# Kernel tuning notes

Hardware: AMD Instinct MI355X
Metric: run time of the kernel (lower is better)

Reference implementation:

```python
import jax, jax.numpy as jnp
import numpy as np
import math

N_STATIONS = 50  # N in [N, 7, 56] causal matrix


def setup_inputs() -> dict:
    key = jax.random.key(0)
    k1, k2, k3, k4 = jax.random.split(key, 4)
    B, L, H, E = 3200, 7, 8, 64
    S, D = 56, 64
    queries = jax.random.normal(k1, (B, L, H, E), dtype=jnp.float32)
    keys = jax.random.normal(k2, (B, S, H, E), dtype=jnp.float32)
    values = jax.random.normal(k3, (B, S, H, D), dtype=jnp.float32)
    # station-specific multiplicative causal matrix in [0, 1]
    attn_mask = jax.random.uniform(k4, (N_STATIONS, L, S), dtype=jnp.float32)
    return {"queries": queries, "keys": keys, "values": values, "attn_mask": attn_mask}


def reference(queries, keys, values, attn_mask):
    B, L, H, E = queries.shape
    S = values.shape[1]
    N = attn_mask.shape[0]  # number of stations; B % N == 0
    ab = B // N  # actual batch size per station group
    scale = 1.0 / math.sqrt(E)
    # raw scores [B, H, L, S]
    scores = jnp.einsum('blhe,bshe->bhls', queries, keys)
    # multiplicative station-specific mask: reshape batch into (ab, N) and
    # broadcast mask [N, L, S] over (ab, H)
    masked = scores.reshape(ab, N, H, L, S) * attn_mask[None, :, None, :, :]
    masked = masked.reshape(B, H, L, S)
    # note: scale is applied AFTER masking, as in the original module
    A = jax.nn.softmax(scale * masked, axis=-1)  # dropout is identity at eval
    V = jnp.einsum('bhls,bshd->blhd', A, values)
    return V
```

## Files before the change

### kernel.cpp

```cpp
#include <hip/hip_runtime.h>
#include <math.h>


__launch_bounds__(64)
__global__ void fullattn_kernel(const float* __restrict__ q,
                                const float* __restrict__ k,
                                const float* __restrict__ v,
                                const float* __restrict__ mask,
                                float* __restrict__ out,
                                int nstations) {
    __shared__ float Klds[56 * 68];

    const int lane = threadIdx.x;
    const int bid  = blockIdx.x;
    const int b    = bid >> 3;
    const int h    = bid & 7;
    const int st   = b % nstations;

    const int kbase = b * 28672 + h * 64;
    const int qbase = b * 3584  + h * 64;

#pragma unroll
    for (int it = 0; it < 14; ++it) {
        const int c  = it * 64 + lane;
        const int s  = c >> 4;
        const int e4 = c & 15;
        const float4 val = *(const float4*)(k + kbase + s * 512 + e4 * 4);
        *(float4*)(&Klds[s * 68 + e4 * 4]) = val;
    }

    const int ml = (lane < 56) ? lane : 55;
    float m[7];
#pragma unroll
    for (int l = 0; l < 7; ++l)
        m[l] = mask[st * 392 + l * 56 + ml] * 0.125f;

    const int sc_row = (lane < 56) ? lane : 55;
    float acc[7];
#pragma unroll
    for (int l = 0; l < 7; ++l) acc[l] = 0.0f;

    const float* qp = q + qbase;
#pragma unroll
    for (int e4 = 0; e4 < 16; ++e4) {
        const float4 kv = *(const float4*)(&Klds[sc_row * 68 + e4 * 4]);
#pragma unroll
        for (int l = 0; l < 7; ++l) {
            const float4 q4 = *(const float4*)(qp + l * 512 + e4 * 4);
            acc[l] = fmaf(q4.x, kv.x, acc[l]);
            acc[l] = fmaf(q4.y, kv.y, acc[l]);
            acc[l] = fmaf(q4.z, kv.z, acc[l]);
            acc[l] = fmaf(q4.w, kv.w, acc[l]);
        }
    }

    float* pbuf = Klds;
    float rdenom[7];
#pragma unroll
    for (int l = 0; l < 7; ++l) {
        float sc = acc[l] * m[l];
        if (lane >= 56) sc = -INFINITY;
        float mx = sc;
#pragma unroll
        for (int off = 32; off >= 1; off >>= 1)
            mx = fmaxf(mx, __shfl_xor(mx, off));
        const float p = __expf(sc - mx);
        float sum = p;
#pragma unroll
        for (int off = 32; off >= 1; off >>= 1)
            sum += __shfl_xor(sum, off);
        pbuf[l * 64 + lane] = p;
        rdenom[l] = 1.0f / sum;
    }

    float facc[7];
#pragma unroll
    for (int l = 0; l < 7; ++l) facc[l] = 0.0f;

#pragma unroll
    for (int s4 = 0; s4 < 14; ++s4) {
        const float vr0 = v[kbase + (s4 * 4 + 0) * 512 + lane];
        const float vr1 = v[kbase + (s4 * 4 + 1) * 512 + lane];
        const float vr2 = v[kbase + (s4 * 4 + 2) * 512 + lane];
        const float vr3 = v[kbase + (s4 * 4 + 3) * 512 + lane];
#pragma unroll
        for (int l = 0; l < 7; ++l) {
            const float4 p4 = *(const float4*)(&pbuf[l * 64 + s4 * 4]);
            facc[l] = fmaf(p4.x, vr0, facc[l]);
            facc[l] = fmaf(p4.y, vr1, facc[l]);
            facc[l] = fmaf(p4.z, vr2, facc[l]);
            facc[l] = fmaf(p4.w, vr3, facc[l]);
        }
    }

#pragma unroll
    for (int l = 0; l < 7; ++l)
        out[qbase + l * 512 + lane] = facc[l] * rdenom[l];
}

extern "C" void kernel_launch(void* const* d_in, const int* in_sizes, int n_in,
                              void* d_out, int out_size, void* d_ws, size_t ws_size,
                              hipStream_t stream) {
    const float* q    = (const float*)d_in[0];
    const float* k    = (const float*)d_in[1];
    const float* v    = (const float*)d_in[2];
    const float* mask = (const float*)d_in[3];
    float* out        = (float*)d_out;

    const int B = in_sizes[0] / (7 * 8 * 64);
    const int nstations = in_sizes[3] / (7 * 56);

    fullattn_kernel<<<dim3(B * 8), dim3(64), 0, stream>>>(q, k, v, mask, out, nstations);
}
```

Measured before the change: 179.7 us.

## Stage K via direct global-to-LDS loads in swizzled halves, two waves per block

Replaces the register-staged K copy into padded LDS with global_load_lds DMA loads, split into two 32-element halves of the head dimension with an XOR swizzle to avoid bank conflicts. This halves the LDS footprint per wave. It also packs two (batch, head) units per 128-thread block, each wave using its own LDS slice. The intent is to cut VGPR traffic and LDS usage so occupancy rises. The cost is an added wait between halves and the assumption that units is even. The loop has no barrier between reusing KL for the second half and the preceding reads, apart from the lgkmcnt wait within a single wave.

```diff
diff --git a/kernel.cpp b/kernel.cpp
--- a/kernel.cpp
+++ b/kernel.cpp
@@ -2,32 +2,30 @@
 #include <math.h>
 
 
-__launch_bounds__(64)
+#define GLDS(gp, lp) __builtin_amdgcn_global_load_lds(                        \
+    (const __attribute__((address_space(1))) void*)(gp),                      \
+    (__attribute__((address_space(3))) void*)(lp), 16, 0, 0)
+
+__launch_bounds__(128)
 __global__ void fullattn_kernel(const float* __restrict__ q,
                                 const float* __restrict__ k,
                                 const float* __restrict__ v,
                                 const float* __restrict__ mask,
                                 float* __restrict__ out,
                                 int nstations) {
-    __shared__ float Klds[56 * 68];
+    __shared__ __align__(16) float KL2[2][1792];
 
-    const int lane = threadIdx.x;
-    const int bid  = blockIdx.x;
-    const int b    = bid >> 3;
-    const int h    = bid & 7;
+    const int lane = threadIdx.x & 63;
+    const int wid  = threadIdx.x >> 6;
+    const int unit = blockIdx.x * 2 + wid;
+    const int b    = unit >> 3;
+    const int h    = unit & 7;
     const int st   = b % nstations;
+
+    float* KL = KL2[wid];
 
     const int kbase = b * 28672 + h * 64;
     const int qbase = b * 3584  + h * 64;
-
-#pragma unroll
-    for (int it = 0; it < 14; ++it) {
-        const int c  = it * 64 + lane;
-        const int s  = c >> 4;
-        const int e4 = c & 15;
-        const float4 val = *(const float4*)(k + kbase + s * 512 + e4 * 4);
-        *(float4*)(&Klds[s * 68 + e4 * 4]) = val;
-    }
 
     const int ml = (lane < 56) ? lane : 55;
     float m[7];
@@ -36,25 +34,41 @@
         m[l] = mask[st * 392 + l * 56 + ml] * 0.125f;
 
     const int sc_row = (lane < 56) ? lane : 55;
+    const int sx     = sc_row & 7;
+    const float* qp  = q + qbase;
+
     float acc[7];
 #pragma unroll
     for (int l = 0; l < 7; ++l) acc[l] = 0.0f;
 
-    const float* qp = q + qbase;
 #pragma unroll
-    for (int e4 = 0; e4 < 16; ++e4) {
-        const float4 kv = *(const float4*)(&Klds[sc_row * 68 + e4 * 4]);
+    for (int half = 0; half < 2; ++half) {
+        const int eoff = half * 32;
 #pragma unroll
-        for (int l = 0; l < 7; ++l) {
-            const float4 q4 = *(const float4*)(qp + l * 512 + e4 * 4);
-            acc[l] = fmaf(q4.x, kv.x, acc[l]);
-            acc[l] = fmaf(q4.y, kv.y, acc[l]);
-            acc[l] = fmaf(q4.z, kv.z, acc[l]);
-            acc[l] = fmaf(q4.w, kv.w, acc[l]);
+        for (int i = 0; i < 7; ++i) {
+            const int f  = i * 64 + lane;
+            const int s  = f >> 3;
+            const int e4 = (f & 7) ^ (s & 7);
+            GLDS(k + kbase + s * 512 + eoff + e4 * 4, (char*)KL + i * 1024);
         }
+        asm volatile("s_waitcnt vmcnt(0)" ::: "memory");
+
+#pragma unroll
+        for (int ee = 0; ee < 8; ++ee) {
+            const float4 kv = *(const float4*)(&KL[sc_row * 32 + ((ee ^ sx) << 2)]);
+#pragma unroll
+            for (int l = 0; l < 7; ++l) {
+                const float4 q4 = *(const float4*)(qp + l * 512 + eoff + ee * 4);
+                acc[l] = fmaf(q4.x, kv.x, acc[l]);
+                acc[l] = fmaf(q4.y, kv.y, acc[l]);
+                acc[l] = fmaf(q4.z, kv.z, acc[l]);
+                acc[l] = fmaf(q4.w, kv.w, acc[l]);
+            }
+        }
+        asm volatile("s_waitcnt lgkmcnt(0)" ::: "memory");
     }
 
-    float* pbuf = Klds;
+    float* pbuf = KL;
     float rdenom[7];
 #pragma unroll
     for (int l = 0; l < 7; ++l) {
@@ -110,5 +124,6 @@
     const int B = in_sizes[0] / (7 * 8 * 64);
     const int nstations = in_sizes[3] / (7 * 56);
 
-    fullattn_kernel<<<dim3(B * 8), dim3(64), 0, stream>>>(q, k, v, mask, out, nstations);
+    const int units = B * 8;
+    fullattn_kernel<<<dim3(units / 2), dim3(128), 0, stream>>>(q, k, v, mask, out, nstations);
 }
```

Measured after the change: 195.9 us. 9.0% more time.

## Store K as fp16 in swizzled LDS and prefetch V into registers early

Applied to the files above, without the earlier changes.

Keys are converted to fp16 and stored in an XOR-swizzled shared buffer, which halves LDS footprint and avoids padding-based bank conflict handling. V rows are loaded into registers in two halves: the first before the softmax and the second after it, so their global latency overlaps with the reductions. The reciprocal uses the hardware rcp builtin. Rounding K to fp16 lowers the precision of the scores, and holding 56 V values per lane raises register pressure.

```diff
diff --git a/kernel.cpp b/kernel.cpp
--- a/kernel.cpp
+++ b/kernel.cpp
@@ -1,6 +1,8 @@
 #include <hip/hip_runtime.h>
 #include <math.h>
 
+
+typedef __attribute__((ext_vector_type(8))) _Float16 half8;
 
 __launch_bounds__(64)
 __global__ void fullattn_kernel(const float* __restrict__ q,
@@ -9,25 +11,16 @@
                                 const float* __restrict__ mask,
                                 float* __restrict__ out,
                                 int nstations) {
-    __shared__ float Klds[56 * 68];
+    __shared__ __align__(16) _Float16 KL[56 * 64];
 
     const int lane = threadIdx.x;
-    const int bid  = blockIdx.x;
-    const int b    = bid >> 3;
-    const int h    = bid & 7;
+    const int unit = blockIdx.x;
+    const int b    = unit >> 3;
+    const int h    = unit & 7;
     const int st   = b % nstations;
 
     const int kbase = b * 28672 + h * 64;
     const int qbase = b * 3584  + h * 64;
-
-#pragma unroll
-    for (int it = 0; it < 14; ++it) {
-        const int c  = it * 64 + lane;
-        const int s  = c >> 4;
-        const int e4 = c & 15;
-        const float4 val = *(const float4*)(k + kbase + s * 512 + e4 * 4);
-        *(float4*)(&Klds[s * 68 + e4 * 4]) = val;
-    }
 
     const int ml = (lane < 56) ? lane : 55;
     float m[7];
@@ -35,26 +28,55 @@
     for (int l = 0; l < 7; ++l)
         m[l] = mask[st * 392 + l * 56 + ml] * 0.125f;
 
-    const int sc_row = (lane < 56) ? lane : 55;
+#pragma unroll
+    for (int i = 0; i < 7; ++i) {
+        const int f = i * 64 + lane;
+        const int s = f >> 3;
+        const int c = f & 7;
+        const float4 a0 = *(const float4*)(k + kbase + s * 512 + c * 8);
+        const float4 a1 = *(const float4*)(k + kbase + s * 512 + c * 8 + 4);
+        half8 hv;
+        hv[0] = (_Float16)a0.x; hv[1] = (_Float16)a0.y;
+        hv[2] = (_Float16)a0.z; hv[3] = (_Float16)a0.w;
+        hv[4] = (_Float16)a1.x; hv[5] = (_Float16)a1.y;
+        hv[6] = (_Float16)a1.z; hv[7] = (_Float16)a1.w;
+        *(half8*)(&KL[s * 64 + 8 * (c ^ (s & 7))]) = hv;
+    }
+
+    const int sr = (lane < 56) ? lane : 55;
+    const int sx = sr & 7;
+    const float* qp = q + qbase;
+
     float acc[7];
 #pragma unroll
     for (int l = 0; l < 7; ++l) acc[l] = 0.0f;
 
-    const float* qp = q + qbase;
 #pragma unroll
-    for (int e4 = 0; e4 < 16; ++e4) {
-        const float4 kv = *(const float4*)(&Klds[sc_row * 68 + e4 * 4]);
+    for (int c = 0; c < 8; ++c) {
+        const half8 kv = *(const half8*)(&KL[sr * 64 + 8 * (c ^ sx)]);
+        float kf[8];
+#pragma unroll
+        for (int j = 0; j < 8; ++j) kf[j] = (float)kv[j];
 #pragma unroll
         for (int l = 0; l < 7; ++l) {
-            const float4 q4 = *(const float4*)(qp + l * 512 + e4 * 4);
-            acc[l] = fmaf(q4.x, kv.x, acc[l]);
-            acc[l] = fmaf(q4.y, kv.y, acc[l]);
-            acc[l] = fmaf(q4.z, kv.z, acc[l]);
-            acc[l] = fmaf(q4.w, kv.w, acc[l]);
+            const float4 q0 = *(const float4*)(qp + l * 512 + c * 8);
+            const float4 q1 = *(const float4*)(qp + l * 512 + c * 8 + 4);
+            acc[l] = fmaf(q0.x, kf[0], acc[l]);
+            acc[l] = fmaf(q0.y, kf[1], acc[l]);
+            acc[l] = fmaf(q0.z, kf[2], acc[l]);
+            acc[l] = fmaf(q0.w, kf[3], acc[l]);
+            acc[l] = fmaf(q1.x, kf[4], acc[l]);
+            acc[l] = fmaf(q1.y, kf[5], acc[l]);
+            acc[l] = fmaf(q1.z, kf[6], acc[l]);
+            acc[l] = fmaf(q1.w, kf[7], acc[l]);
         }
     }
 
-    float* pbuf = Klds;
+    float vb0[28];
+#pragma unroll
+    for (int i = 0; i < 28; ++i) vb0[i] = v[kbase + i * 512 + lane];
+
+    float* pbuf = (float*)KL;
     float rdenom[7];
 #pragma unroll
     for (int l = 0; l < 7; ++l) {
@@ -70,26 +92,37 @@
         for (int off = 32; off >= 1; off >>= 1)
             sum += __shfl_xor(sum, off);
         pbuf[l * 64 + lane] = p;
-        rdenom[l] = 1.0f / sum;
+        rdenom[l] = __builtin_amdgcn_rcpf(sum);
     }
+
+    float vb1[28];
+#pragma unroll
+    for (int i = 0; i < 28; ++i) vb1[i] = v[kbase + (28 + i) * 512 + lane];
 
     float facc[7];
 #pragma unroll
     for (int l = 0; l < 7; ++l) facc[l] = 0.0f;
 
 #pragma unroll
-    for (int s4 = 0; s4 < 14; ++s4) {
-        const float vr0 = v[kbase + (s4 * 4 + 0) * 512 + lane];
-        const float vr1 = v[kbase + (s4 * 4 + 1) * 512 + lane];
-        const float vr2 = v[kbase + (s4 * 4 + 2) * 512 + lane];
-        const float vr3 = v[kbase + (s4 * 4 + 3) * 512 + lane];
+    for (int s4 = 0; s4 < 7; ++s4) {
 #pragma unroll
         for (int l = 0; l < 7; ++l) {
             const float4 p4 = *(const float4*)(&pbuf[l * 64 + s4 * 4]);
-            facc[l] = fmaf(p4.x, vr0, facc[l]);
-            facc[l] = fmaf(p4.y, vr1, facc[l]);
-            facc[l] = fmaf(p4.z, vr2, facc[l]);
-            facc[l] = fmaf(p4.w, vr3, facc[l]);
+            facc[l] = fmaf(p4.x, vb0[s4 * 4 + 0], facc[l]);
+            facc[l] = fmaf(p4.y, vb0[s4 * 4 + 1], facc[l]);
+            facc[l] = fmaf(p4.z, vb0[s4 * 4 + 2], facc[l]);
+            facc[l] = fmaf(p4.w, vb0[s4 * 4 + 3], facc[l]);
+        }
+    }
+#pragma unroll
+    for (int s4 = 0; s4 < 7; ++s4) {
+#pragma unroll
+        for (int l = 0; l < 7; ++l) {
+            const float4 p4 = *(const float4*)(&pbuf[l * 64 + 28 + s4 * 4]);
+            facc[l] = fmaf(p4.x, vb1[s4 * 4 + 0], facc[l]);
+            facc[l] = fmaf(p4.y, vb1[s4 * 4 + 1], facc[l]);
+            facc[l] = fmaf(p4.z, vb1[s4 * 4 + 2], facc[l]);
+            facc[l] = fmaf(p4.w, vb1[s4 * 4 + 3], facc[l]);
         }
     }
 
```

After: 168.9 us. -6.0%, faster.
